# Optimization experiments

Measured on AMD Instinct MI355X. Metric: run time of the kernel, lower is better.

The kernel has to match this reference:

```python
import jax, jax.numpy as jnp
import numpy as np

H = 12          # heads in the ViT blocks
D = 768         # model dim (hard-coded in the module)
DFF = 3072      # mlp hidden = 4*D
ADIM = 64       # adapter bottleneck dim
L = 32          # num_latents
EPS = 1e-6      # timm ViT LayerNorm eps


def _ln(x, g, b):
    m = jnp.mean(x, axis=-1, keepdims=True)
    v = jnp.var(x, axis=-1, keepdims=True)
    return (x - m) * jax.lax.rsqrt(v + EPS) * g + b


def _quick_gelu(x):
    return x * jax.nn.sigmoid(1.702 * x)


def _sh_attn(q, k, v):
    # single-head attention used by fusion(); scale = C**-0.5 with C = full dim
    C = q.shape[-1]
    a = jax.nn.softmax(jnp.einsum('bnc,bmc->bnm', q, k) * (C ** -0.5), axis=-1)
    return jnp.einsum('bnm,bmc->bnc', a, v)


def _mhsa(x, qkv_w, qkv_b, proj_w, proj_b):
    B, N, C = x.shape
    Dh = C // H
    qkv = (x @ qkv_w.T + qkv_b).reshape(B, N, 3, H, Dh).transpose(2, 0, 3, 1, 4)
    q, k, v = qkv[0], qkv[1], qkv[2]                       # [B,H,N,Dh]
    a = jax.nn.softmax(jnp.einsum('bhnd,bhmd->bhnm', q, k) * (Dh ** -0.5), axis=-1)
    o = jnp.einsum('bhnm,bhmd->bhnd', a, v).transpose(0, 2, 1, 3).reshape(B, N, C)
    return o @ proj_w.T + proj_b


def _stream(t, ln1_g, ln1_b, qkv_w, qkv_b, proj_w, proj_b,
            ln2_g, ln2_b, fc1_w, fc1_b, fc2_w, fc2_b,
            down_w, down_b, up_w, up_b, scale):
    t = t + _mhsa(_ln(t, ln1_g, ln1_b), qkv_w, qkv_b, proj_w, proj_b)
    h = _ln(t, ln2_g, ln2_b)
    mlp = jax.nn.gelu(h @ fc1_w.T + fc1_b, approximate=False) @ fc2_w.T + fc2_b
    adapter = (_quick_gelu(h @ down_w.T + down_b) @ up_w.T + up_b) * scale
    return t + mlp + adapter


def setup_inputs() -> dict:
    key = jax.random.key(0)
    ks = iter(jax.random.split(key, 64))
    f32 = jnp.float32
    def rn(shape, std=0.02):
        return (jax.random.normal(next(ks), shape, dtype=f32) * std)
    inp = {
        'x': jax.random.normal(next(ks), (16, 512, 768), dtype=f32),
        'y': jax.random.normal(next(ks), (16, 196, 768), dtype=f32),
        'latents': rn((1, L, D)),
        'scale_a': jnp.full((1,), 0.5, f32),
        'scale_v': jnp.full((1,), 0.5, f32),
    }
    for p in ('spec', 'rgb'):
        inp.update({
            f'{p}_ln1_g': jnp.ones((D,), f32), f'{p}_ln1_b': jnp.zeros((D,), f32),
            f'{p}_qkv_w': rn((3 * D, D)), f'{p}_qkv_b': jnp.zeros((3 * D,), f32),
            f'{p}_proj_w': rn((D, D)), f'{p}_proj_b': jnp.zeros((D,), f32),
            f'{p}_ln2_g': jnp.ones((D,), f32), f'{p}_ln2_b': jnp.zeros((D,), f32),
            f'{p}_fc1_w': rn((DFF, D)), f'{p}_fc1_b': jnp.zeros((DFF,), f32),
            f'{p}_fc2_w': rn((D, DFF)), f'{p}_fc2_b': jnp.zeros((D,), f32),
            f'{p}_down_w': rn((ADIM, D)), f'{p}_down_b': jnp.zeros((ADIM,), f32),
            f'{p}_up_w': rn((D, ADIM)), f'{p}_up_b': jnp.zeros((D,), f32),
            f'{p}_scale': jnp.ones((1,), f32),
        })
    return inp


def reference(x, y, latents, scale_a, scale_v,
              spec_ln1_g, spec_ln1_b, spec_qkv_w, spec_qkv_b, spec_proj_w, spec_proj_b,
              spec_ln2_g, spec_ln2_b, spec_fc1_w, spec_fc1_b, spec_fc2_w, spec_fc2_b,
              spec_down_w, spec_down_b, spec_up_w, spec_up_b, spec_scale,
              rgb_ln1_g, rgb_ln1_b, rgb_qkv_w, rgb_qkv_b, rgb_proj_w, rgb_proj_b,
              rgb_ln2_g, rgb_ln2_b, rgb_fc1_w, rgb_fc1_b, rgb_fc2_w, rgb_fc2_b,
              rgb_down_w, rgb_down_b, rgb_up_w, rgb_up_b, rgb_scale):
    B = x.shape[0]
    # --- fusion via latent bottleneck (single-head attention) ---
    concat_ = jnp.concatenate((x, y), axis=1)                 # [B, Na+Nv, D]
    lat = jnp.broadcast_to(latents, (B, L, D))
    fused = _sh_attn(lat, concat_, concat_)                   # [B, L, D]
    x = x + scale_a * _sh_attn(x, fused, fused)
    y = y + scale_v * _sh_attn(y, fused, fused)
    # --- per-stream transformer block + adapter (dropout = eval/identity) ---
    x = _stream(x, spec_ln1_g, spec_ln1_b, spec_qkv_w, spec_qkv_b, spec_proj_w, spec_proj_b,
                spec_ln2_g, spec_ln2_b, spec_fc1_w, spec_fc1_b, spec_fc2_w, spec_fc2_b,
                spec_down_w, spec_down_b, spec_up_w, spec_up_b, spec_scale)
    y = _stream(y, rgb_ln1_g, rgb_ln1_b, rgb_qkv_w, rgb_qkv_b, rgb_proj_w, rgb_proj_b,
                rgb_ln2_g, rgb_ln2_b, rgb_fc1_w, rgb_fc1_b, rgb_fc2_w, rgb_fc2_b,
                rgb_down_w, rgb_down_b, rgb_up_w, rgb_up_b, rgb_scale)
    return (x, y)
```

## Files before the change

kernel.cpp:

```cpp
#include <hip/hip_runtime.h>
#include <hip/hip_bf16.h>


#define H_HEADS 12
#define DMODEL 768
#define DFF 3072
#define ADIM 64
#define NLAT 32
#define BATCH 16
#define NA 512
#define NV 196

typedef __hip_bfloat16 bf16;
using bf16x8 = __attribute__((ext_vector_type(8))) short;
using f32x4  = __attribute__((ext_vector_type(4))) float;

static __device__ __forceinline__ float bf2f(bf16 v) { return __bfloat162float(v); }
static __device__ __forceinline__ float bflo(unsigned u) { return __uint_as_float(u << 16); }
static __device__ __forceinline__ float bfhi(unsigned u) { return __uint_as_float(u & 0xffff0000u); }
static __device__ __forceinline__ float ld1(const float* p) { return *p; }
static __device__ __forceinline__ float ld1(const bf16* p) { return bf2f(*p); }
static __device__ __forceinline__ float4 ld4(const float* p) { return *(const float4*)p; }
static __device__ __forceinline__ float4 ld4(const bf16* p) {
    ushort4 u = *(const ushort4*)p;
    return make_float4(bflo(u.x), bflo(u.y), bflo(u.z), bflo(u.w));
}
static __device__ __forceinline__ unsigned short f2bf_bits(float v) {
    unsigned u = __float_as_uint(v);
    return (unsigned short)((u + 0x7fffu + ((u >> 16) & 1u)) >> 16);
}

#define GLD_LDS16(gp, lp) __builtin_amdgcn_global_load_lds( \
    (const __attribute__((address_space(1))) void*)(gp), \
    (__attribute__((address_space(3))) void*)(lp), 16, 0, 0)

__global__ void detect_dtype_kernel(const unsigned short* __restrict__ x, int* __restrict__ flag)
{
    if (threadIdx.x == 0 && blockIdx.x == 0) {
        int big = 0;
        for (int i = 0; i < 2048; i++) {
            unsigned e = (x[i] >> 7) & 0xFF;
            if (e >= 0x90) big++;
        }
        flag[0] = (big > 16) ? 1 : 0;
    }
}

template<typename TIn>
static __device__ __forceinline__ void fusion_latents_body(
    const TIn* __restrict__ x, const TIn* __restrict__ y,
    const TIn* __restrict__ lat, float* __restrict__ fused)
{
    const int b = blockIdx.x >> 5;
    const int l = blockIdx.x & 31;
    const int tid = threadIdx.x;
    const int NTOT = NA + NV;

    __shared__ float q[DMODEL];
    __shared__ float sc[NA + NV];
    __shared__ float red[4];

    for (int d = tid; d < DMODEL; d += 256) q[d] = ld1(lat + l * DMODEL + d);
    __syncthreads();

    for (int n = tid; n < NTOT; n += 256) {
        const TIn* rowp = (n < NA)
            ? x + ((size_t)(b * NA + n)) * DMODEL
            : y + ((size_t)(b * NV + (n - NA))) * DMODEL;
        float s = 0.f;
        for (int d = 0; d < DMODEL; d += 4) {
            float4 rv = ld4(rowp + d);
            s += q[d] * rv.x + q[d + 1] * rv.y + q[d + 2] * rv.z + q[d + 3] * rv.w;
        }
        sc[n] = s * 0.03608439182435161f;
    }
    __syncthreads();

    float mx = -1e30f;
    for (int n = tid; n < NTOT; n += 256) mx = fmaxf(mx, sc[n]);
    #pragma unroll
    for (int off = 32; off; off >>= 1) mx = fmaxf(mx, __shfl_xor(mx, off));
    if ((tid & 63) == 0) red[tid >> 6] = mx;
    __syncthreads();
    mx = fmaxf(fmaxf(red[0], red[1]), fmaxf(red[2], red[3]));
    __syncthreads();
    float ds = 0.f;
    for (int n = tid; n < NTOT; n += 256) { float e = __expf(sc[n] - mx); sc[n] = e; ds += e; }
    #pragma unroll
    for (int off = 32; off; off >>= 1) ds += __shfl_xor(ds, off);
    __syncthreads();
    if ((tid & 63) == 0) red[tid >> 6] = ds;
    __syncthreads();
    const float inv = 1.0f / (red[0] + red[1] + red[2] + red[3]);

    float a0 = 0.f, a1 = 0.f, a2 = 0.f;
    for (int n = 0; n < NTOT; n++) {
        const TIn* rowp = (n < NA)
            ? x + ((size_t)(b * NA + n)) * DMODEL
            : y + ((size_t)(b * NV + (n - NA))) * DMODEL;
        const float pn = sc[n];
        a0 += pn * ld1(rowp + tid);
        a1 += pn * ld1(rowp + tid + 256);
        a2 += pn * ld1(rowp + tid + 512);
    }
    float* o = fused + (size_t)blockIdx.x * DMODEL;
    o[tid] = a0 * inv; o[tid + 256] = a1 * inv; o[tid + 512] = a2 * inv;
}

__global__ __launch_bounds__(256)
void fusion_latents_kernel(const int* __restrict__ flag, const void* x, const void* y,
                           const void* lat, float* __restrict__ fused)
{
    if (flag[0]) fusion_latents_body<float>((const float*)x, (const float*)y, (const float*)lat, fused);
    else         fusion_latents_body<bf16>((const bf16*)x, (const bf16*)y, (const bf16*)lat, fused);
}

template<typename TIn>
static __device__ __forceinline__ void attend_fused_body(
    const TIn* __restrict__ t, const float* __restrict__ fused,
    const TIn* __restrict__ scale_p, bf16* __restrict__ out, int Npb)
{
    const int tid = threadIdx.x;
    const int gid = blockIdx.x;
    const int b = gid / Npb;
    const TIn* row = t + (size_t)gid * DMODEL;
    const float* fb = fused + (size_t)b * NLAT * DMODEL;

    __shared__ float q[DMODEL];
    __shared__ float p[NLAT];

    for (int d = tid; d < DMODEL; d += 256) q[d] = ld1(row + d);
    __syncthreads();

    const int g = tid >> 3, li = tid & 7;
    float s = 0.f;
    const float* fr = fb + (size_t)g * DMODEL;
    for (int d = li; d < DMODEL; d += 8) s += q[d] * fr[d];
    s += __shfl_xor(s, 1); s += __shfl_xor(s, 2); s += __shfl_xor(s, 4);
    if (li == 0) p[g] = s * 0.03608439182435161f;
    __syncthreads();

    float mx = -1e30f;
    #pragma unroll
    for (int l = 0; l < NLAT; l++) mx = fmaxf(mx, p[l]);
    float w[NLAT];
    float den = 0.f;
    #pragma unroll
    for (int l = 0; l < NLAT; l++) { w[l] = __expf(p[l] - mx); den += w[l]; }
    const float sA = ld1(scale_p) / den;

    float a0 = 0.f, a1 = 0.f, a2 = 0.f;
    #pragma unroll
    for (int l = 0; l < NLAT; l++) {
        const float* fv = fb + (size_t)l * DMODEL;
        a0 += w[l] * fv[tid];
        a1 += w[l] * fv[tid + 256];
        a2 += w[l] * fv[tid + 512];
    }
    bf16* o = out + (size_t)gid * DMODEL;
    o[tid]       = __float2bfloat16(q[tid]       + sA * a0);
    o[tid + 256] = __float2bfloat16(q[tid + 256] + sA * a1);
    o[tid + 512] = __float2bfloat16(q[tid + 512] + sA * a2);
}

__global__ __launch_bounds__(256)
void attend_fused_kernel(const int* __restrict__ flag, const void* t, const float* __restrict__ fused,
                         const void* scale_p, bf16* __restrict__ out, int Npb)
{
    if (flag[0]) attend_fused_body<float>((const float*)t, fused, (const float*)scale_p, out, Npb);
    else         attend_fused_body<bf16>((const bf16*)t, fused, (const bf16*)scale_p, out, Npb);
}

template<typename TW>
static __device__ __forceinline__ void ln_body(
    const bf16* __restrict__ in, const TW* __restrict__ g,
    const TW* __restrict__ bta, bf16* __restrict__ out)
{
    const int tid = threadIdx.x;
    const bf16* p = in + (size_t)blockIdx.x * DMODEL;
    const float v0 = bf2f(p[tid]), v1 = bf2f(p[tid + 256]), v2 = bf2f(p[tid + 512]);
    float s = v0 + v1 + v2;
    float sq = v0 * v0 + v1 * v1 + v2 * v2;
    #pragma unroll
    for (int off = 32; off; off >>= 1) { s += __shfl_xor(s, off); sq += __shfl_xor(sq, off); }
    __shared__ float rs[4], rq[4];
    if ((tid & 63) == 0) { rs[tid >> 6] = s; rq[tid >> 6] = sq; }
    __syncthreads();
    s = rs[0] + rs[1] + rs[2] + rs[3];
    sq = rq[0] + rq[1] + rq[2] + rq[3];
    const float mean = s * (1.0f / DMODEL);
    const float var = sq * (1.0f / DMODEL) - mean * mean;
    const float r = rsqrtf(var + 1e-6f);
    bf16* o = out + (size_t)blockIdx.x * DMODEL;
    o[tid]       = __float2bfloat16((v0 - mean) * r * ld1(g + tid)       + ld1(bta + tid));
    o[tid + 256] = __float2bfloat16((v1 - mean) * r * ld1(g + tid + 256) + ld1(bta + tid + 256));
    o[tid + 512] = __float2bfloat16((v2 - mean) * r * ld1(g + tid + 512) + ld1(bta + tid + 512));
}

__global__ __launch_bounds__(256)
void ln_kernel(const int* __restrict__ flag, const bf16* __restrict__ in,
               const void* g, const void* b, bf16* __restrict__ out)
{
    if (flag[0]) ln_body<float>(in, (const float*)g, (const float*)b, out);
    else         ln_body<bf16>(in, (const bf16*)g, (const bf16*)b, out);
}

__global__ __launch_bounds__(256)
void flash_attn_kernel(const bf16* __restrict__ qkv, bf16* __restrict__ o, int Npb)
{
    const int tid = threadIdx.x;
    const int wv = tid >> 6, lane = tid & 63;
    const int l15 = lane & 15, q4 = lane >> 4;
    const int qt = blockIdx.x, h = blockIdx.y, bb = blockIdx.z;
    const int nkv = (Npb + 63) >> 6;
    const size_t tokbase = (size_t)bb * Npb;

    __shared__ __align__(16) short Ks[64 * 64];
    __shared__ __align__(16) short Vt[64 * 64];
    __shared__ __align__(16) short Ps[4][16 * 64];

    const int qr = min(qt * 64 + wv * 16 + l15, Npb - 1);
    const bf16* qp = qkv + (tokbase + qr) * 2304 + h * 64;
    const bf16x8 qf0 = *(const bf16x8*)(const void*)(qp + q4 * 8);
    const bf16x8 qf1 = *(const bf16x8*)(const void*)(qp + 32 + q4 * 8);

    f32x4 Oa[4] = {};
    float mrow[4], lrow[4];
    #pragma unroll
    for (int i = 0; i < 4; i++) { mrow[i] = -1e30f; lrow[i] = 0.f; }

    for (int kv = 0; kv < nkv; kv++) {
        const int kv0 = kv * 64;
        __syncthreads();
        #pragma unroll
        for (int inst = 0; inst < 2; inst++) {
            const int s = inst * 256 + tid;
            const int row = s >> 3, pos = s & 7;
            const int c = pos ^ (row & 7);
            const int krc = min(kv0 + row, Npb - 1);
            GLD_LDS16(qkv + (tokbase + krc) * 2304 + DMODEL + h * 64 + c * 8, &Ks[s * 8]);
        }
        {
            const int r = tid >> 2;
            const int f0 = (tid & 3) * 16;
            const int krc = min(kv0 + r, Npb - 1);
            const short* vp = (const short*)(qkv + (tokbase + krc) * 2304 + 2 * DMODEL + h * 64 + f0);
            short vb[16];
            *(uint4*)&vb[0] = *(const uint4*)vp;
            *(uint4*)&vb[8] = *(const uint4*)(vp + 8);
            const int chunk = r >> 3, r7 = r & 7;
            #pragma unroll
            for (int j = 0; j < 16; j++) {
                const int feat = f0 + j;
                Vt[feat * 64 + (chunk ^ (feat & 7)) * 8 + r7] = vb[j];
            }
        }
        __syncthreads();

        f32x4 s4[4] = {};
        #pragma unroll
        for (int kk = 0; kk < 2; kk++) {
            const bf16x8 qf = kk ? qf1 : qf0;
            const int c = kk * 4 + q4;
            #pragma unroll
            for (int g = 0; g < 4; g++) {
                const int r = g * 16 + l15;
                const bf16x8 kf = *(const bf16x8*)(const void*)&Ks[r * 64 + (c ^ (r & 7)) * 8];
                s4[g] = __builtin_amdgcn_mfma_f32_16x16x32_bf16(qf, kf, s4[g], 0, 0, 0);
            }
        }
        float tmax[4];
        #pragma unroll
        for (int i = 0; i < 4; i++) tmax[i] = -1e30f;
        #pragma unroll
        for (int g = 0; g < 4; g++) {
            const bool valid = (kv0 + g * 16 + l15) < Npb;
            #pragma unroll
            for (int i = 0; i < 4; i++) {
                const float v = s4[g][i] * 0.125f;
                s4[g][i] = valid ? v : -1e30f;
                tmax[i] = fmaxf(tmax[i], s4[g][i]);
            }
        }
        #pragma unroll
        for (int off = 1; off < 16; off <<= 1)
            #pragma unroll
            for (int i = 0; i < 4; i++) tmax[i] = fmaxf(tmax[i], __shfl_xor(tmax[i], off));
        float alpha[4], rsum[4];
        #pragma unroll
        for (int i = 0; i < 4; i++) {
            const float mn = fmaxf(mrow[i], tmax[i]);
            alpha[i] = __expf(mrow[i] - mn);
            mrow[i] = mn;
            rsum[i] = 0.f;
        }
        #pragma unroll
        for (int g = 0; g < 4; g++) {
            const int cc = g * 16 + l15;
            const int chunk = cc >> 3;
            #pragma unroll
            for (int i = 0; i < 4; i++) {
                const int r = q4 * 4 + i;
                const float p = __expf(s4[g][i] - mrow[i]);
                rsum[i] += p;
                Ps[wv][r * 64 + (chunk ^ (r & 7)) * 8 + (cc & 7)] = (short)f2bf_bits(p);
            }
        }
        #pragma unroll
        for (int off = 1; off < 16; off <<= 1)
            #pragma unroll
            for (int i = 0; i < 4; i++) rsum[i] += __shfl_xor(rsum[i], off);
        #pragma unroll
        for (int i = 0; i < 4; i++) lrow[i] = lrow[i] * alpha[i] + rsum[i];
        #pragma unroll
        for (int g = 0; g < 4; g++)
            #pragma unroll
            for (int i = 0; i < 4; i++) Oa[g][i] *= alpha[i];

        #pragma unroll
        for (int kk = 0; kk < 2; kk++) {
            const int c = kk * 4 + q4;
            const bf16x8 pf = *(const bf16x8*)(const void*)&Ps[wv][l15 * 64 + (c ^ (l15 & 7)) * 8];
            #pragma unroll
            for (int g = 0; g < 4; g++) {
                const int feat = g * 16 + l15;
                const bf16x8 vf = *(const bf16x8*)(const void*)&Vt[feat * 64 + (c ^ (feat & 7)) * 8];
                Oa[g] = __builtin_amdgcn_mfma_f32_16x16x32_bf16(pf, vf, Oa[g], 0, 0, 0);
            }
        }
    }

    float inv[4];
    #pragma unroll
    for (int i = 0; i < 4; i++) inv[i] = 1.0f / lrow[i];
    #pragma unroll
    for (int g = 0; g < 4; g++) {
        const int colo = h * 64 + g * 16 + l15;
        #pragma unroll
        for (int i = 0; i < 4; i++) {
            const int rowg = qt * 64 + wv * 16 + q4 * 4 + i;
            if (rowg < Npb)
                o[(tokbase + rowg) * DMODEL + colo] = __float2bfloat16(Oa[g][i] * inv[i]);
        }
    }
}

template<typename TW, int ACT, bool RES, bool SCALE>
static __device__ __forceinline__ void gemm_body(
    const bf16* __restrict__ A, const TW* __restrict__ W, const TW* __restrict__ bias,
    const bf16* __restrict__ resid, const TW* __restrict__ scale_p, void* __restrict__ C,
    bool cf32, int row_off, int M, int N, int K, short* As, short* Bs)
{
    const int tid = threadIdx.x;
    const int lane = tid & 63;
    const int wv = tid >> 6;
    const int l15 = lane & 15, q4 = lane >> 4;
    const int m0 = blockIdx.y * 128, n0 = blockIdx.x * 128;
    const int wm = (wv & 1) * 64, wn = (wv >> 1) * 64;

    f32x4 acc[4][4] = {};

    for (int k0 = 0; k0 < K; k0 += 32) {
        __syncthreads();
        #pragma unroll
        for (int inst = 0; inst < 2; inst++) {
            const int s = inst * 256 + tid;
            const int row = s >> 2, pos = s & 3;
            const int c = pos ^ ((row >> 1) & 3);
            const int ra = min(m0 + row, M - 1);
            const int rb = min(n0 + row, N - 1);
            GLD_LDS16(A + (size_t)ra * K + k0 + c * 8, &As[s * 8]);
            if (sizeof(TW) == 2) {
                GLD_LDS16((const bf16*)W + (size_t)rb * K + k0 + c * 8, &Bs[s * 8]);
            } else {
                const float* wp = (const float*)W + (size_t)rb * K + k0 + c * 8;
                const float4 w0 = *(const float4*)wp;
                const float4 w1 = *(const float4*)(wp + 4);
                unsigned short hb[8];
                hb[0] = f2bf_bits(w0.x); hb[1] = f2bf_bits(w0.y);
                hb[2] = f2bf_bits(w0.z); hb[3] = f2bf_bits(w0.w);
                hb[4] = f2bf_bits(w1.x); hb[5] = f2bf_bits(w1.y);
                hb[6] = f2bf_bits(w1.z); hb[7] = f2bf_bits(w1.w);
                *(uint4*)&Bs[s * 8] = *(const uint4*)hb;
            }
        }
        __syncthreads();

        bf16x8 af[4], bfr[4];
        #pragma unroll
        for (int f = 0; f < 4; f++) {
            const int r = wm + f * 16 + l15;
            af[f] = *(const bf16x8*)(const void*)&As[r * 32 + (q4 ^ ((r >> 1) & 3)) * 8];
            const int rn = wn + f * 16 + l15;
            bfr[f] = *(const bf16x8*)(const void*)&Bs[rn * 32 + (q4 ^ ((rn >> 1) & 3)) * 8];
        }
        #pragma unroll
        for (int f = 0; f < 4; f++)
            #pragma unroll
            for (int g = 0; g < 4; g++)
                acc[f][g] = __builtin_amdgcn_mfma_f32_16x16x32_bf16(af[f], bfr[g], acc[f][g], 0, 0, 0);
    }

    const float sc = SCALE ? ld1(scale_p) : 1.0f;
    #pragma unroll
    for (int g = 0; g < 4; g++) {
        const int colg = n0 + wn + g * 16 + l15;
        if (colg >= N) continue;
        const float bv = ld1(bias + colg);
        #pragma unroll
        for (int f = 0; f < 4; f++) {
            const int rowb = m0 + wm + f * 16 + q4 * 4;
            #pragma unroll
            for (int i = 0; i < 4; i++) {
                const int rowg = rowb + i;
                if (rowg >= M) continue;
                float v = acc[f][g][i] + bv;
                if (ACT == 1) v = 0.5f * v * (1.0f + erff(v * 0.70710678118654752f));
                else if (ACT == 2) v = v / (1.0f + __expf(-1.702f * v));
                if (SCALE) v *= sc;
                const size_t idx = (size_t)rowg * N + colg;
                if (RES) v += bf2f(resid[idx]);
                const size_t sidx = (size_t)(rowg + row_off) * N + colg;
                if (cf32) ((float*)C)[sidx] = v;
                else ((bf16*)C)[sidx] = __float2bfloat16(v);
            }
        }
    }
}

template<int ACT, bool RES, bool SCALE>
__global__ __launch_bounds__(256)
void mfma_gemm_kernel(const int* __restrict__ flag, const bf16* __restrict__ A,
                      const void* __restrict__ W, const void* __restrict__ bias,
                      const bf16* __restrict__ resid, const void* __restrict__ sp,
                      void* __restrict__ C, int final_out, int row_off, int M, int N, int K)
{
    __shared__ __align__(16) short As[128 * 32];
    __shared__ __align__(16) short Bs[128 * 32];
    if (flag[0])
        gemm_body<float, ACT, RES, SCALE>(A, (const float*)W, (const float*)bias, resid,
                                          (const float*)sp, C, final_out != 0, row_off, M, N, K, As, Bs);
    else
        gemm_body<bf16, ACT, RES, SCALE>(A, (const bf16*)W, (const bf16*)bias, resid,
                                         (const bf16*)sp, C, false, row_off, M, N, K, As, Bs);
}

struct SW {
    const void *ln1_g, *ln1_b, *qkv_w, *qkv_b, *proj_w, *proj_b,
               *ln2_g, *ln2_b, *fc1_w, *fc1_b, *fc2_w, *fc2_b,
               *down_w, *down_b, *up_w, *up_b, *scale;
};

static void run_stream(const int* flag, bf16* t0, int M, int Npb, int nb, const SW& w,
                       bf16* h, bf16* big, bf16* ah, void* out, int out_row_off, hipStream_t s)
{
    const dim3 g768((DMODEL + 127) / 128, (M + 127) / 128);
    const dim3 g2304((2304 + 127) / 128, (M + 127) / 128);
    const dim3 g3072((DFF + 127) / 128, (M + 127) / 128);
    const dim3 g64((ADIM + 127) / 128, (M + 127) / 128);

    ln_kernel<<<M, 256, 0, s>>>(flag, t0, w.ln1_g, w.ln1_b, h);
    mfma_gemm_kernel<0, false, false><<<g2304, 256, 0, s>>>(
        flag, h, w.qkv_w, w.qkv_b, nullptr, nullptr, big, 0, 0, M, 2304, DMODEL);
    flash_attn_kernel<<<dim3((Npb + 63) / 64, H_HEADS, nb), 256, 0, s>>>(big, h, Npb);
    mfma_gemm_kernel<0, true, false><<<g768, 256, 0, s>>>(
        flag, h, w.proj_w, w.proj_b, t0, nullptr, t0, 0, 0, M, DMODEL, DMODEL);
    ln_kernel<<<M, 256, 0, s>>>(flag, t0, w.ln2_g, w.ln2_b, h);
    mfma_gemm_kernel<1, false, false><<<g3072, 256, 0, s>>>(
        flag, h, w.fc1_w, w.fc1_b, nullptr, nullptr, big, 0, 0, M, DFF, DMODEL);
    mfma_gemm_kernel<2, false, false><<<g64, 256, 0, s>>>(
        flag, h, w.down_w, w.down_b, nullptr, nullptr, ah, 0, 0, M, ADIM, DMODEL);
    mfma_gemm_kernel<0, true, false><<<g768, 256, 0, s>>>(
        flag, big, w.fc2_w, w.fc2_b, t0, nullptr, t0, 0, 0, M, DMODEL, DFF);
    mfma_gemm_kernel<0, true, true><<<g768, 256, 0, s>>>(
        flag, ah, w.up_w, w.up_b, t0, w.scale, out, 1, out_row_off, M, DMODEL, ADIM);
}

extern "C" void kernel_launch(void* const* d_in, const int* in_sizes, int n_in,
                              void* d_out, int out_size, void* d_ws, size_t ws_size,
                              hipStream_t stream)
{
    SW sw, rw;
    auto fill = [&](SW& s, int base) {
        s.ln1_g = d_in[base + 0];  s.ln1_b = d_in[base + 1];
        s.qkv_w = d_in[base + 2];  s.qkv_b = d_in[base + 3];
        s.proj_w = d_in[base + 4]; s.proj_b = d_in[base + 5];
        s.ln2_g = d_in[base + 6];  s.ln2_b = d_in[base + 7];
        s.fc1_w = d_in[base + 8];  s.fc1_b = d_in[base + 9];
        s.fc2_w = d_in[base + 10]; s.fc2_b = d_in[base + 11];
        s.down_w = d_in[base + 12]; s.down_b = d_in[base + 13];
        s.up_w = d_in[base + 14];  s.up_b = d_in[base + 15];
        s.scale = d_in[base + 16];
    };
    fill(sw, 5);
    fill(rw, 22);

    const int Mx = BATCH * NA;
    const int My = BATCH * NV;

    const size_t need_big = 256 + 1572864ull + (size_t)Mx * DMODEL * 2 + (size_t)My * DMODEL * 2
                          + (size_t)Mx * DMODEL * 2 + (size_t)Mx * DFF * 2 + (size_t)Mx * ADIM * 2;
    const bool big_ws = ws_size >= need_big;
    const int hrows = big_ws ? Mx : My;

    int* flag = (int*)d_ws;
    char* base = (char*)d_ws + 256;
    float* fused = (float*)base;              base += (size_t)BATCH * NLAT * DMODEL * 4;
    bf16* x1 = (bf16*)base;                   base += (size_t)Mx * DMODEL * 2;
    bf16* y1 = (bf16*)base;                   base += (size_t)My * DMODEL * 2;
    bf16* h  = (bf16*)base;                   base += (size_t)hrows * DMODEL * 2;
    bf16* big = (bf16*)base;                  base += (size_t)hrows * DFF * 2;
    bf16* ah = (bf16*)base;

    detect_dtype_kernel<<<1, 64, 0, stream>>>((const unsigned short*)d_in[0], flag);

    fusion_latents_kernel<<<BATCH * NLAT, 256, 0, stream>>>(flag, d_in[0], d_in[1], d_in[2], fused);
    attend_fused_kernel<<<BATCH * NA, 256, 0, stream>>>(flag, d_in[0], fused, d_in[3], x1, NA);
    attend_fused_kernel<<<BATCH * NV, 256, 0, stream>>>(flag, d_in[1], fused, d_in[4], y1, NV);

    if (big_ws) {
        run_stream(flag, x1, Mx, NA, BATCH, sw, h, big, ah, d_out, 0, stream);
    } else {
        const int MCH = 2048;
        for (int c = 0; c < Mx / MCH; c++)
            run_stream(flag, x1 + (size_t)c * MCH * DMODEL, MCH, NA, MCH / NA, sw,
                       h, big, ah, d_out, c * MCH, stream);
    }
    run_stream(flag, y1, My, NV, BATCH, rw, h, big, ah, d_out, Mx, stream);
}
```

Before: 1.431 ms.

## Split latent fusion attention into pack, MFMA score GEMM, softmax and tiled weighted-sum kernels

Replaces the monolithic per-(batch, latent) fusion kernel, which re-read every concat row with scalar dot products, with four stages. A pack kernel converts x, y and the latents to bf16. The MFMA GEMM computes the latent scores into fp32, a small softmax kernel normalises them, and a tiled LDS kernel forms the weighted sum over concat rows. The fused latents are now stored in bf16 rather than fp32, which halves traffic in attend_fused and costs some precision. It adds a pack pass over the inputs and workspace that overlaps the stream buffers, and the GEMM uses only 32 of its 128 output columns.

```diff
diff --git a/kernel.cpp b/kernel.cpp
--- a/kernel.cpp
+++ b/kernel.cpp
@@ -10,6 +10,8 @@
 #define BATCH 16
 #define NA 512
 #define NV 196
+#define NTOT 708
+#define MCAT (BATCH * NTOT)
 
 typedef __hip_bfloat16 bf16;
 using bf16x8 = __attribute__((ext_vector_type(8))) short;
@@ -17,14 +19,8 @@
 
 static __device__ __forceinline__ float bf2f(bf16 v) { return __bfloat162float(v); }
 static __device__ __forceinline__ float bflo(unsigned u) { return __uint_as_float(u << 16); }
-static __device__ __forceinline__ float bfhi(unsigned u) { return __uint_as_float(u & 0xffff0000u); }
 static __device__ __forceinline__ float ld1(const float* p) { return *p; }
 static __device__ __forceinline__ float ld1(const bf16* p) { return bf2f(*p); }
-static __device__ __forceinline__ float4 ld4(const float* p) { return *(const float4*)p; }
-static __device__ __forceinline__ float4 ld4(const bf16* p) {
-    ushort4 u = *(const ushort4*)p;
-    return make_float4(bflo(u.x), bflo(u.y), bflo(u.z), bflo(u.w));
-}
 static __device__ __forceinline__ unsigned short f2bf_bits(float v) {
     unsigned u = __float_as_uint(v);
     return (unsigned short)((u + 0x7fffu + ((u >> 16) & 1u)) >> 16);
@@ -43,88 +39,137 @@
             if (e >= 0x90) big++;
         }
         flag[0] = (big > 16) ? 1 : 0;
+        flag[1] = 0;
     }
 }
 
 template<typename TIn>
-static __device__ __forceinline__ void fusion_latents_body(
-    const TIn* __restrict__ x, const TIn* __restrict__ y,
-    const TIn* __restrict__ lat, float* __restrict__ fused)
-{
-    const int b = blockIdx.x >> 5;
-    const int l = blockIdx.x & 31;
+static __device__ __forceinline__ void pack_body(
+    const TIn* __restrict__ x, const TIn* __restrict__ y, const TIn* __restrict__ lat,
+    bf16* __restrict__ Cc, bf16* __restrict__ Lb)
+{
+    const int r = blockIdx.x, tid = threadIdx.x;
+    const TIn* src;
+    bf16* dst;
+    if (r < MCAT) {
+        const int b = r / NTOT, n = r - b * NTOT;
+        src = (n < NA) ? x + ((size_t)(b * NA + n)) * DMODEL
+                       : y + ((size_t)(b * NV + (n - NA))) * DMODEL;
+        dst = Cc + (size_t)r * DMODEL;
+    } else {
+        src = lat + (size_t)(r - MCAT) * DMODEL;
+        dst = Lb + (size_t)(r - MCAT) * DMODEL;
+    }
+    dst[tid]       = __float2bfloat16(ld1(src + tid));
+    dst[tid + 256] = __float2bfloat16(ld1(src + tid + 256));
+    dst[tid + 512] = __float2bfloat16(ld1(src + tid + 512));
+}
+
+__global__ __launch_bounds__(256)
+void pack_concat_kernel(const int* __restrict__ flag, const void* x, const void* y,
+                        const void* lat, bf16* __restrict__ Cc, bf16* __restrict__ Lb)
+{
+    if (flag[0]) pack_body<float>((const float*)x, (const float*)y, (const float*)lat, Cc, Lb);
+    else         pack_body<bf16>((const bf16*)x, (const bf16*)y, (const bf16*)lat, Cc, Lb);
+}
+
+__global__ __launch_bounds__(64)
+void fusion_softmax_kernel(const float* __restrict__ scores, float* __restrict__ P)
+{
+    const int b = blockIdx.x >> 5, l = blockIdx.x & 31, lane = threadIdx.x;
+    const float* sp = scores + (size_t)b * NTOT * NLAT + l;
+    float v[12];
+    float mx = -1e30f;
+    #pragma unroll
+    for (int i = 0; i < 12; i++) {
+        const int n = lane + i * 64;
+        v[i] = (n < NTOT) ? sp[(size_t)n * NLAT] * 0.03608439182435161f : -1e30f;
+        mx = fmaxf(mx, v[i]);
+    }
+    #pragma unroll
+    for (int off = 32; off; off >>= 1) mx = fmaxf(mx, __shfl_xor(mx, off));
+    float den = 0.f;
+    #pragma unroll
+    for (int i = 0; i < 12; i++) { v[i] = __expf(v[i] - mx); den += v[i]; }
+    #pragma unroll
+    for (int off = 32; off; off >>= 1) den += __shfl_xor(den, off);
+    const float inv = 1.0f / den;
+    float* op = P + ((size_t)b * NLAT + l) * 768;
+    #pragma unroll
+    for (int i = 0; i < 12; i++) {
+        const int n = lane + i * 64;
+        op[n] = (n < NTOT) ? v[i] * inv : 0.f;
+    }
+}
+
+__global__ __launch_bounds__(256)
+void fusion_wsum_kernel(const bf16* __restrict__ Cc, const float* __restrict__ P,
+                        bf16* __restrict__ fused)
+{
+    const int b = blockIdx.y, d0 = blockIdx.x * 128;
     const int tid = threadIdx.x;
-    const int NTOT = NA + NV;
-
-    __shared__ float q[DMODEL];
-    __shared__ float sc[NA + NV];
-    __shared__ float red[4];
-
-    for (int d = tid; d < DMODEL; d += 256) q[d] = ld1(lat + l * DMODEL + d);
-    __syncthreads();
-
-    for (int n = tid; n < NTOT; n += 256) {
-        const TIn* rowp = (n < NA)
-            ? x + ((size_t)(b * NA + n)) * DMODEL
-            : y + ((size_t)(b * NV + (n - NA))) * DMODEL;
-        float s = 0.f;
-        for (int d = 0; d < DMODEL; d += 4) {
-            float4 rv = ld4(rowp + d);
-            s += q[d] * rv.x + q[d + 1] * rv.y + q[d + 2] * rv.z + q[d + 3] * rv.w;
-        }
-        sc[n] = s * 0.03608439182435161f;
-    }
-    __syncthreads();
-
-    float mx = -1e30f;
-    for (int n = tid; n < NTOT; n += 256) mx = fmaxf(mx, sc[n]);
-    #pragma unroll
-    for (int off = 32; off; off >>= 1) mx = fmaxf(mx, __shfl_xor(mx, off));
-    if ((tid & 63) == 0) red[tid >> 6] = mx;
-    __syncthreads();
-    mx = fmaxf(fmaxf(red[0], red[1]), fmaxf(red[2], red[3]));
-    __syncthreads();
-    float ds = 0.f;
-    for (int n = tid; n < NTOT; n += 256) { float e = __expf(sc[n] - mx); sc[n] = e; ds += e; }
-    #pragma unroll
-    for (int off = 32; off; off >>= 1) ds += __shfl_xor(ds, off);
-    __syncthreads();
-    if ((tid & 63) == 0) red[tid >> 6] = ds;
-    __syncthreads();
-    const float inv = 1.0f / (red[0] + red[1] + red[2] + red[3]);
-
-    float a0 = 0.f, a1 = 0.f, a2 = 0.f;
-    for (int n = 0; n < NTOT; n++) {
-        const TIn* rowp = (n < NA)
-            ? x + ((size_t)(b * NA + n)) * DMODEL
-            : y + ((size_t)(b * NV + (n - NA))) * DMODEL;
-        const float pn = sc[n];
-        a0 += pn * ld1(rowp + tid);
-        a1 += pn * ld1(rowp + tid + 256);
-        a2 += pn * ld1(rowp + tid + 512);
-    }
-    float* o = fused + (size_t)blockIdx.x * DMODEL;
-    o[tid] = a0 * inv; o[tid + 256] = a1 * inv; o[tid + 512] = a2 * inv;
-}
-
-__global__ __launch_bounds__(256)
-void fusion_latents_kernel(const int* __restrict__ flag, const void* x, const void* y,
-                           const void* lat, float* __restrict__ fused)
-{
-    if (flag[0]) fusion_latents_body<float>((const float*)x, (const float*)y, (const float*)lat, fused);
-    else         fusion_latents_body<bf16>((const bf16*)x, (const bf16*)y, (const bf16*)lat, fused);
+    const int lg = tid >> 5, dg = tid & 31;
+    const int l0 = lg * 4;
+
+    __shared__ float Ct[64][132];
+    __shared__ float Ps[32][68];
+
+    float acc[4][4] = {};
+
+    for (int nc = 0; nc < 12; nc++) {
+        const int n0 = nc * 64;
+        __syncthreads();
+        #pragma unroll
+        for (int it = 0; it < 8; it++) {
+            const int idx = it * 1024 + tid * 4;
+            const int r = idx >> 7, c = idx & 127;
+            const int gn = n0 + r;
+            float4 v = make_float4(0.f, 0.f, 0.f, 0.f);
+            if (gn < NTOT) {
+                const ushort4 u = *(const ushort4*)(Cc + ((size_t)(b * NTOT + gn)) * DMODEL + d0 + c);
+                v = make_float4(bflo(u.x), bflo(u.y), bflo(u.z), bflo(u.w));
+            }
+            Ct[r][c] = v.x; Ct[r][c + 1] = v.y; Ct[r][c + 2] = v.z; Ct[r][c + 3] = v.w;
+        }
+        {
+            const int l = tid >> 3, off = (tid & 7) * 8;
+            const float* pp = P + ((size_t)b * NLAT + l) * 768 + n0 + off;
+            const float4 p0 = *(const float4*)pp;
+            const float4 p1 = *(const float4*)(pp + 4);
+            Ps[l][off] = p0.x; Ps[l][off + 1] = p0.y; Ps[l][off + 2] = p0.z; Ps[l][off + 3] = p0.w;
+            Ps[l][off + 4] = p1.x; Ps[l][off + 5] = p1.y; Ps[l][off + 6] = p1.z; Ps[l][off + 7] = p1.w;
+        }
+        __syncthreads();
+
+        for (int n = 0; n < 64; n++) {
+            const float4 v = *(const float4*)&Ct[n][dg * 4];
+            #pragma unroll
+            for (int i = 0; i < 4; i++) {
+                const float p = Ps[l0 + i][n];
+                acc[i][0] += p * v.x; acc[i][1] += p * v.y;
+                acc[i][2] += p * v.z; acc[i][3] += p * v.w;
+            }
+        }
+    }
+
+    #pragma unroll
+    for (int i = 0; i < 4; i++) {
+        bf16* op = fused + ((size_t)b * NLAT + l0 + i) * DMODEL + d0 + dg * 4;
+        #pragma unroll
+        for (int j = 0; j < 4; j++) op[j] = __float2bfloat16(acc[i][j]);
+    }
 }
 
 template<typename TIn>
 static __device__ __forceinline__ void attend_fused_body(
-    const TIn* __restrict__ t, const float* __restrict__ fused,
+    const TIn* __restrict__ t, const bf16* __restrict__ fused,
     const TIn* __restrict__ scale_p, bf16* __restrict__ out, int Npb)
 {
     const int tid = threadIdx.x;
     const int gid = blockIdx.x;
     const int b = gid / Npb;
     const TIn* row = t + (size_t)gid * DMODEL;
-    const float* fb = fused + (size_t)b * NLAT * DMODEL;
+    const bf16* fb = fused + (size_t)b * NLAT * DMODEL;
 
     __shared__ float q[DMODEL];
     __shared__ float p[NLAT];
@@ -134,8 +179,8 @@
 
     const int g = tid >> 3, li = tid & 7;
     float s = 0.f;
-    const float* fr = fb + (size_t)g * DMODEL;
-    for (int d = li; d < DMODEL; d += 8) s += q[d] * fr[d];
+    const bf16* fr = fb + (size_t)g * DMODEL;
+    for (int d = li; d < DMODEL; d += 8) s += q[d] * bf2f(fr[d]);
     s += __shfl_xor(s, 1); s += __shfl_xor(s, 2); s += __shfl_xor(s, 4);
     if (li == 0) p[g] = s * 0.03608439182435161f;
     __syncthreads();
@@ -152,10 +197,10 @@
     float a0 = 0.f, a1 = 0.f, a2 = 0.f;
     #pragma unroll
     for (int l = 0; l < NLAT; l++) {
-        const float* fv = fb + (size_t)l * DMODEL;
-        a0 += w[l] * fv[tid];
-        a1 += w[l] * fv[tid + 256];
-        a2 += w[l] * fv[tid + 512];
+        const bf16* fv = fb + (size_t)l * DMODEL;
+        a0 += w[l] * bf2f(fv[tid]);
+        a1 += w[l] * bf2f(fv[tid + 256]);
+        a2 += w[l] * bf2f(fv[tid + 512]);
     }
     bf16* o = out + (size_t)gid * DMODEL;
     o[tid]       = __float2bfloat16(q[tid]       + sA * a0);
@@ -164,7 +209,7 @@
 }
 
 __global__ __launch_bounds__(256)
-void attend_fused_kernel(const int* __restrict__ flag, const void* t, const float* __restrict__ fused,
+void attend_fused_kernel(const int* __restrict__ flag, const void* t, const bf16* __restrict__ fused,
                          const void* scale_p, bf16* __restrict__ out, int Npb)
 {
     if (flag[0]) attend_fused_body<float>((const float*)t, fused, (const float*)scale_p, out, Npb);
@@ -406,7 +451,7 @@
     for (int g = 0; g < 4; g++) {
         const int colg = n0 + wn + g * 16 + l15;
         if (colg >= N) continue;
-        const float bv = ld1(bias + colg);
+        const float bv = bias ? ld1(bias + colg) : 0.f;
         #pragma unroll
         for (int f = 0; f < 4; f++) {
             const int rowb = m0 + wm + f * 16 + q4 * 4;
@@ -433,16 +478,17 @@
 void mfma_gemm_kernel(const int* __restrict__ flag, const bf16* __restrict__ A,
                       const void* __restrict__ W, const void* __restrict__ bias,
                       const bf16* __restrict__ resid, const void* __restrict__ sp,
-                      void* __restrict__ C, int final_out, int row_off, int M, int N, int K)
+                      void* __restrict__ C, int out_mode, int row_off, int M, int N, int K)
 {
     __shared__ __align__(16) short As[128 * 32];
     __shared__ __align__(16) short Bs[128 * 32];
+    const bool cf32 = (out_mode == 2) || (out_mode == 1 && flag[0] != 0);
     if (flag[0])
         gemm_body<float, ACT, RES, SCALE>(A, (const float*)W, (const float*)bias, resid,
-                                          (const float*)sp, C, final_out != 0, row_off, M, N, K, As, Bs);
+                                          (const float*)sp, C, cf32, row_off, M, N, K, As, Bs);
     else
         gemm_body<bf16, ACT, RES, SCALE>(A, (const bf16*)W, (const bf16*)bias, resid,
-                                         (const bf16*)sp, C, false, row_off, M, N, K, As, Bs);
+                                         (const bf16*)sp, C, cf32, row_off, M, N, K, As, Bs);
 }
 
 struct SW {
@@ -498,23 +544,34 @@
     const int Mx = BATCH * NA;
     const int My = BATCH * NV;
 
-    const size_t need_big = 256 + 1572864ull + (size_t)Mx * DMODEL * 2 + (size_t)My * DMODEL * 2
-                          + (size_t)Mx * DMODEL * 2 + (size_t)Mx * DFF * 2 + (size_t)Mx * ADIM * 2;
-    const bool big_ws = ws_size >= need_big;
-    const int hrows = big_ws ? Mx : My;
-
     int* flag = (int*)d_ws;
     char* base = (char*)d_ws + 256;
-    float* fused = (float*)base;              base += (size_t)BATCH * NLAT * DMODEL * 4;
-    bf16* x1 = (bf16*)base;                   base += (size_t)Mx * DMODEL * 2;
-    bf16* y1 = (bf16*)base;                   base += (size_t)My * DMODEL * 2;
-    bf16* h  = (bf16*)base;                   base += (size_t)hrows * DMODEL * 2;
-    bf16* big = (bf16*)base;                  base += (size_t)hrows * DFF * 2;
-    bf16* ah = (bf16*)base;
+    bf16* x1 = (bf16*)base;                base += (size_t)Mx * DMODEL * 2;
+    bf16* y1 = (bf16*)base;                base += (size_t)My * DMODEL * 2;
+    bf16* fused = (bf16*)base;             base += (size_t)BATCH * NLAT * DMODEL * 2;
+    char* un = base;
+
+    bf16* Cc = (bf16*)un;
+    bf16* Lb = (bf16*)(un + (size_t)MCAT * DMODEL * 2);
+    float* scores = (float*)(un + (size_t)(MCAT + 64) * DMODEL * 2);
+    float* P = (float*)((char*)scores + (size_t)MCAT * NLAT * 4 + 256);
+
+    const size_t stream_need_big = ((size_t)Mx * DMODEL + (size_t)Mx * DFF + (size_t)Mx * ADIM) * 2;
+    const size_t fixed = 256 + ((size_t)Mx * DMODEL + (size_t)My * DMODEL + (size_t)BATCH * NLAT * DMODEL) * 2;
+    const bool big_ws = ws_size >= fixed + stream_need_big;
+    const int hrows = big_ws ? Mx : My;
+    bf16* h  = (bf16*)un;
+    bf16* big = h + (size_t)hrows * DMODEL;
+    bf16* ah = big + (size_t)hrows * DFF;
 
     detect_dtype_kernel<<<1, 64, 0, stream>>>((const unsigned short*)d_in[0], flag);
 
-    fusion_latents_kernel<<<BATCH * NLAT, 256, 0, stream>>>(flag, d_in[0], d_in[1], d_in[2], fused);
+    pack_concat_kernel<<<MCAT + NLAT, 256, 0, stream>>>(flag, d_in[0], d_in[1], d_in[2], Cc, Lb);
+    mfma_gemm_kernel<0, false, false><<<dim3(1, (MCAT + 127) / 128), 256, 0, stream>>>(
+        flag + 1, Cc, Lb, nullptr, nullptr, nullptr, scores, 2, 0, MCAT, NLAT, DMODEL);
+    fusion_softmax_kernel<<<BATCH * NLAT, 64, 0, stream>>>(scores, P);
+    fusion_wsum_kernel<<<dim3(DMODEL / 128, BATCH), 256, 0, stream>>>(Cc, P, fused);
+
     attend_fused_kernel<<<BATCH * NA, 256, 0, stream>>>(flag, d_in[0], fused, d_in[3], x1, NA);
     attend_fused_kernel<<<BATCH * NV, 256, 0, stream>>>(flag, d_in[1], fused, d_in[4], y1, NV);
 
```

New measurement: 1.293 ms. 1.11x faster.
